# Performance work log

Hardware: AMD Instinct MI355X
Metric: run time of the kernel (lower is better)

Reference implementation:

```python
import jax, jax.numpy as jnp
import numpy as np

B, L, D = 8, 2048, 1024


def setup_inputs() -> dict:
    key = jax.random.key(0)
    kq, kk, kv, km = jax.random.split(key, 4)
    q = jax.random.normal(kq, (B, L, D), dtype=jnp.float32)
    k = jax.random.normal(kk, (B, L, D), dtype=jnp.float32)
    v = jax.random.normal(kv, (B, L, D), dtype=jnp.float32)
    rep_mask = jax.random.randint(km, (B, L, 1), 0, 2, dtype=jnp.int32)
    return {"q": q, "k": k, "v": v, "rep_mask": rep_mask}


def reference(q, k, v, rep_mask):
    # rep_mask: (B, L, 1) binary -> tiled pair mask (B, L, L)
    b, l, _ = rep_mask.shape
    m = rep_mask.astype(jnp.float32)
    mask = m.reshape(b, l, 1) * m.reshape(b, 1, l)  # (B, L, L)

    # scores: (B, L1, L2)
    attn = jnp.einsum('bqd,bkd->bqk', q, k)

    # custom masked softmax (faithful to original: mask applied pre-max and post-exp)
    masked_vec = attn * mask
    max_vec = jnp.max(masked_vec, axis=2, keepdims=True)
    masked_exps = jnp.exp(masked_vec - max_vec) * mask
    masked_sums = jnp.sum(masked_exps, axis=2, keepdims=True)
    masked_sums = masked_sums + (masked_sums == 0).astype(jnp.float32)  # avoid 0/0 rows
    attn = masked_exps / (masked_sums + 1e-20)

    out = jnp.einsum('bqk,bkd->bqd', attn, v)
    return out
```

## Files before the change

### kernel.cpp

```cpp
#include <hip/hip_runtime.h>
#include <cstdint>
#include <cstddef>

#define BB 8
#define LL 2048
#define DD 1024
#define KT 8

typedef _Float16 f16;
typedef _Float16 f16x4 __attribute__((ext_vector_type(4)));
typedef _Float16 f16x8 __attribute__((ext_vector_type(8)));
typedef float f32x4 __attribute__((ext_vector_type(4)));

__device__ __forceinline__ void gload_lds16(const void* g, void* l) {
  __builtin_amdgcn_global_load_lds(
      (const __attribute__((address_space(1))) void*)g,
      (__attribute__((address_space(3))) void*)l, 16, 0, 0);
}

__global__ void cvt_kernel(const float* __restrict__ src, f16* __restrict__ dst, int n) {
  const int t = blockIdx.x * blockDim.x + threadIdx.x;
  const int stride = gridDim.x * blockDim.x;
  for (int i = t * 4; i < n; i += stride * 4) {
    const float4 v = *(const float4*)(src + i);
    f16x4 o;
    o[0] = (f16)v.x; o[1] = (f16)v.y; o[2] = (f16)v.z; o[3] = (f16)v.w;
    *(f16x4*)(dst + i) = o;
  }
}

__global__ void vtrans_kernel(const float* __restrict__ v, f16* __restrict__ vt) {
  __shared__ float tile[32][33];
  const int b = blockIdx.z;
  const int k0 = blockIdx.x * 32, d0 = blockIdx.y * 32;
  const int tx = threadIdx.x & 31, ty0 = threadIdx.x >> 5;
#pragma unroll
  for (int i = 0; i < 4; ++i) {
    int ty = ty0 + i * 8;
    tile[ty][tx] = v[((size_t)b * LL + k0 + ty) * DD + d0 + tx];
  }
  __syncthreads();
#pragma unroll
  for (int i = 0; i < 4; ++i) {
    int ty = ty0 + i * 8;
    vt[((size_t)b * DD + d0 + ty) * LL + k0 + tx] = (f16)tile[tx][ty];
  }
}

template <int MODE>
__global__ __launch_bounds__(256, 2) void qk_kernel(
    const f16* __restrict__ Q16, const f16* __restrict__ K16,
    const int* __restrict__ rep, float* __restrict__ part,
    const float* __restrict__ MR, f16* __restrict__ P16) {
  __shared__ __align__(16) f16 Qs[64 * 32];
  __shared__ __align__(16) f16 Ks[256 * 32];
  __shared__ float mrow[64];
  __shared__ float mcol[256];
  __shared__ float MRs[128];
  __shared__ float pm[256];
  __shared__ float pz[256];

  const int kt = blockIdx.x, qt = blockIdx.y, b = blockIdx.z;
  const int q0 = qt * 64, k0 = kt * 256;
  const int tid = threadIdx.x;
  const int w = tid >> 6, l = tid & 63;

  mcol[tid] = (float)rep[(size_t)b * LL + k0 + tid];
  if (tid < 64) mrow[tid] = (float)rep[(size_t)b * LL + q0 + tid];
  if (MODE == 1 && tid < 128) MRs[tid] = MR[((size_t)b * LL + q0) * 2 + tid];

  const int rl = l >> 2, jc = l & 3;
  const int jsrc = jc ^ ((rl >> 1) & 3);
  const f16* qsrc = Q16 + ((size_t)b * LL + q0 + w * 16 + rl) * DD + jsrc * 8;
  const f16* ksrc = K16 + ((size_t)b * LL + k0 + w * 64 + rl) * DD + jsrc * 8;

  f32x4 acc[4][4] = {};
  const int lo16 = l & 15, hi = l >> 4;

  for (int ds = 0; ds < 32; ++ds) {
    gload_lds16(qsrc + ds * 32, &Qs[w * 16 * 32]);
    gload_lds16(ksrc + ds * 32,            &Ks[(w * 64) * 32]);
    gload_lds16(ksrc + 16 * DD + ds * 32,  &Ks[(w * 64 + 16) * 32]);
    gload_lds16(ksrc + 32 * DD + ds * 32,  &Ks[(w * 64 + 32) * 32]);
    gload_lds16(ksrc + 48 * DD + ds * 32,  &Ks[(w * 64 + 48) * 32]);
    __syncthreads();
    f16x8 af[4];
#pragma unroll
    for (int qf = 0; qf < 4; ++qf) {
      int r = qf * 16 + lo16;
      af[qf] = *(const f16x8*)&Qs[r * 32 + ((hi ^ ((r >> 1) & 3)) << 3)];
    }
#pragma unroll
    for (int kf = 0; kf < 4; ++kf) {
      int rk = w * 64 + kf * 16 + lo16;
      f16x8 bf = *(const f16x8*)&Ks[rk * 32 + ((hi ^ ((rk >> 1) & 3)) << 3)];
#pragma unroll
      for (int qf = 0; qf < 4; ++qf)
        acc[qf][kf] = __builtin_amdgcn_mfma_f32_16x16x32_f16(af[qf], bf, acc[qf][kf], 0, 0, 0);
    }
    __syncthreads();
  }

  float mkv[4];
#pragma unroll
  for (int kf = 0; kf < 4; ++kf) mkv[kf] = mcol[w * 64 + kf * 16 + lo16];

  if (MODE == 0) {
#pragma unroll
    for (int qf = 0; qf < 4; ++qf) {
#pragma unroll
      for (int r = 0; r < 4; ++r) {
        const int row = qf * 16 + hi * 4 + r;
        const float mqv = mrow[row];
        float v0 = acc[qf][0][r] * mqv * mkv[0];
        float v1 = acc[qf][1][r] * mqv * mkv[1];
        float v2 = acc[qf][2][r] * mqv * mkv[2];
        float v3 = acc[qf][3][r] * mqv * mkv[3];
        float mx = fmaxf(fmaxf(v0, v1), fmaxf(v2, v3));
#pragma unroll
        for (int s = 1; s < 16; s <<= 1) mx = fmaxf(mx, __shfl_xor(mx, s, 64));
        float zz = 0.f;
        zz += (mqv * mkv[0] != 0.f) ? __expf(v0 - mx) : 0.f;
        zz += (mqv * mkv[1] != 0.f) ? __expf(v1 - mx) : 0.f;
        zz += (mqv * mkv[2] != 0.f) ? __expf(v2 - mx) : 0.f;
        zz += (mqv * mkv[3] != 0.f) ? __expf(v3 - mx) : 0.f;
#pragma unroll
        for (int s = 1; s < 16; s <<= 1) zz += __shfl_xor(zz, s, 64);
        if (lo16 == 0) { pm[w * 64 + row] = mx; pz[w * 64 + row] = zz; }
      }
    }
    __syncthreads();
    if (tid < 64) {
      float m0 = pm[tid], m1 = pm[64 + tid], m2 = pm[128 + tid], m3 = pm[192 + tid];
      float M4 = fmaxf(fmaxf(m0, m1), fmaxf(m2, m3));
      float Z4 = pz[tid] * __expf(m0 - M4) + pz[64 + tid] * __expf(m1 - M4) +
                 pz[128 + tid] * __expf(m2 - M4) + pz[192 + tid] * __expf(m3 - M4);
      size_t base = (((size_t)b * LL + q0 + tid) * KT + kt) * 2;
      part[base] = M4;
      part[base + 1] = Z4;
    }
  } else {
#pragma unroll
    for (int qf = 0; qf < 4; ++qf) {
#pragma unroll
      for (int r = 0; r < 4; ++r) {
        const int row = qf * 16 + hi * 4 + r;
        const float mqv = mrow[row];
        const float Mv = MRs[row * 2], Rv = MRs[row * 2 + 1];
#pragma unroll
        for (int kf = 0; kf < 4; ++kf) {
          float p = 0.f;
          if (mqv * mkv[kf] != 0.f) p = __expf(acc[qf][kf][r] - Mv) * Rv;
          P16[((size_t)b * LL + q0 + row) * LL + (k0 + w * 64 + kf * 16 + lo16)] = (f16)p;
        }
      }
    }
  }
}

__global__ void combine_kernel(const float* __restrict__ part, float* __restrict__ MR) {
  const int row = blockIdx.x * blockDim.x + threadIdx.x;
  const float* p = part + (size_t)row * KT * 2;
  float M = p[0];
#pragma unroll
  for (int t = 1; t < KT; ++t) M = fmaxf(M, p[2 * t]);
  float Z = 0.f;
#pragma unroll
  for (int t = 0; t < KT; ++t) Z += p[2 * t + 1] * __expf(p[2 * t] - M);
  float Zf = Z + ((Z == 0.f) ? 1.f : 0.f) + 1e-20f;
  MR[(size_t)row * 2] = M;
  MR[(size_t)row * 2 + 1] = 1.f / Zf;
}

__global__ __launch_bounds__(256, 2) void pv_kernel(
    const f16* __restrict__ P16, const f16* __restrict__ V16T, float* __restrict__ out) {
  __shared__ __align__(16) f16 Ps[64 * 32];
  __shared__ __align__(16) f16 Vs[4][64 * 32];
  const int dt = blockIdx.x, qt = blockIdx.y, b = blockIdx.z;
  const int q0 = qt * 64, d0 = dt * 256;
  const int tid = threadIdx.x, w = tid >> 6, l = tid & 63;
  const int rl = l >> 2, jc = l & 3, jsrc = jc ^ ((rl >> 1) & 3);
  const int lo16 = l & 15, hi = l >> 4;

  const f16* psrc = P16 + ((size_t)b * LL + q0 + w * 16 + rl) * LL + jsrc * 8;
  const f16* vsrc = V16T + ((size_t)b * DD + d0 + w * 64 + rl) * LL + jsrc * 8;

  f32x4 acc[4][4] = {};

  for (int ks = 0; ks < 64; ++ks) {
    gload_lds16(psrc + ks * 32, &Ps[w * 16 * 32]);
    gload_lds16(vsrc + ks * 32,           &Vs[w][0]);
    gload_lds16(vsrc + 16 * LL + ks * 32, &Vs[w][16 * 32]);
    gload_lds16(vsrc + 32 * LL + ks * 32, &Vs[w][32 * 32]);
    gload_lds16(vsrc + 48 * LL + ks * 32, &Vs[w][48 * 32]);
    __syncthreads();
    f16x8 af[4];
#pragma unroll
    for (int qf = 0; qf < 4; ++qf) {
      int r = qf * 16 + lo16;
      af[qf] = *(const f16x8*)&Ps[r * 32 + ((hi ^ ((r >> 1) & 3)) << 3)];
    }
#pragma unroll
    for (int df = 0; df < 4; ++df) {
      int rv = df * 16 + lo16;
      f16x8 bf = *(const f16x8*)&Vs[w][rv * 32 + ((hi ^ ((rv >> 1) & 3)) << 3)];
#pragma unroll
      for (int qf = 0; qf < 4; ++qf)
        acc[qf][df] = __builtin_amdgcn_mfma_f32_16x16x32_f16(af[qf], bf, acc[qf][df], 0, 0, 0);
    }
    __syncthreads();
  }
#pragma unroll
  for (int qf = 0; qf < 4; ++qf)
#pragma unroll
    for (int df = 0; df < 4; ++df)
#pragma unroll
      for (int r = 0; r < 4; ++r) {
        int row = qf * 16 + hi * 4 + r;
        int col = d0 + w * 64 + df * 16 + lo16;
        out[((size_t)b * LL + q0 + row) * DD + col] = acc[qf][df][r];
      }
}

extern "C" void kernel_launch(void* const* d_in, const int* in_sizes, int n_in,
                              void* d_out, int out_size, void* d_ws, size_t ws_size,
                              hipStream_t stream) {
  const float* q = (const float*)d_in[0];
  const float* k = (const float*)d_in[1];
  const float* v = (const float*)d_in[2];
  const int* rep = (const int*)d_in[3];
  float* out = (float*)d_out;

  char* ws = (char*)d_ws;
  f16* Q16 = (f16*)(ws);
  f16* K16 = (f16*)(ws + 33554432);
  f16* V16T = (f16*)(ws + 67108864);
  f16* P16 = (f16*)(ws + 100663296);
  float* part = (float*)(ws + 167772160);
  float* MR = (float*)(ws + 168820736);

  const int n = BB * LL * DD;
  cvt_kernel<<<2048, 256, 0, stream>>>(q, Q16, n);
  cvt_kernel<<<2048, 256, 0, stream>>>(k, K16, n);
  vtrans_kernel<<<dim3(LL / 32, DD / 32, BB), 256, 0, stream>>>(v, V16T);
  qk_kernel<0><<<dim3(KT, LL / 64, BB), 256, 0, stream>>>(Q16, K16, rep, part, nullptr, nullptr);
  combine_kernel<<<BB * LL / 256, 256, 0, stream>>>(part, MR);
  qk_kernel<1><<<dim3(KT, LL / 64, BB), 256, 0, stream>>>(Q16, K16, rep, nullptr, MR, P16);
  pv_kernel<<<dim3(DD / 256, LL / 64, BB), 256, 0, stream>>>(P16, V16T, out);
}
```

Measured before the change: 526.9 us.

## Fuse QK passes with tile-local softmax and rescale in PV; double-buffer loads

The second QK GEMM pass is removed. The single QK kernel now writes exp(score minus the tile-local max) to P16, along with per-tile max and sum partials. The PV kernel computes a per-row, per-key-tile correction factor from the partials and the combined max/reciprocal-sum, and multiplies the P fragments by it before the MFMA. Both GEMM loops also gain double-buffered LDS staging, so the next K-slice load overlaps the current compute. This saves a full QK GEMM, at the cost of extra LDS, an extra reduction barrier, and f16 rounding of the correction factors.

```diff
diff --git a/kernel.cpp b/kernel.cpp
--- a/kernel.cpp
+++ b/kernel.cpp
@@ -47,18 +47,17 @@
   }
 }
 
-template <int MODE>
 __global__ __launch_bounds__(256, 2) void qk_kernel(
     const f16* __restrict__ Q16, const f16* __restrict__ K16,
     const int* __restrict__ rep, float* __restrict__ part,
-    const float* __restrict__ MR, f16* __restrict__ P16) {
-  __shared__ __align__(16) f16 Qs[64 * 32];
-  __shared__ __align__(16) f16 Ks[256 * 32];
+    f16* __restrict__ P16) {
+  __shared__ __align__(16) f16 Qs[2][64 * 32];
+  __shared__ __align__(16) f16 Ks[2][256 * 32];
   __shared__ float mrow[64];
   __shared__ float mcol[256];
-  __shared__ float MRs[128];
   __shared__ float pm[256];
   __shared__ float pz[256];
+  __shared__ float mr64[64];
 
   const int kt = blockIdx.x, qt = blockIdx.y, b = blockIdx.z;
   const int q0 = qt * 64, k0 = kt * 256;
@@ -67,7 +66,6 @@
 
   mcol[tid] = (float)rep[(size_t)b * LL + k0 + tid];
   if (tid < 64) mrow[tid] = (float)rep[(size_t)b * LL + q0 + tid];
-  if (MODE == 1 && tid < 128) MRs[tid] = MR[((size_t)b * LL + q0) * 2 + tid];
 
   const int rl = l >> 2, jc = l & 3;
   const int jsrc = jc ^ ((rl >> 1) & 3);
@@ -77,84 +75,94 @@
   f32x4 acc[4][4] = {};
   const int lo16 = l & 15, hi = l >> 4;
 
+  auto stage = [&](int buf, int ds) {
+    gload_lds16(qsrc + ds * 32, &Qs[buf][w * 16 * 32]);
+    gload_lds16(ksrc + ds * 32,           &Ks[buf][(w * 64) * 32]);
+    gload_lds16(ksrc + 16 * DD + ds * 32, &Ks[buf][(w * 64 + 16) * 32]);
+    gload_lds16(ksrc + 32 * DD + ds * 32, &Ks[buf][(w * 64 + 32) * 32]);
+    gload_lds16(ksrc + 48 * DD + ds * 32, &Ks[buf][(w * 64 + 48) * 32]);
+  };
+
+  stage(0, 0);
+  __syncthreads();
+  int cur = 0;
   for (int ds = 0; ds < 32; ++ds) {
-    gload_lds16(qsrc + ds * 32, &Qs[w * 16 * 32]);
-    gload_lds16(ksrc + ds * 32,            &Ks[(w * 64) * 32]);
-    gload_lds16(ksrc + 16 * DD + ds * 32,  &Ks[(w * 64 + 16) * 32]);
-    gload_lds16(ksrc + 32 * DD + ds * 32,  &Ks[(w * 64 + 32) * 32]);
-    gload_lds16(ksrc + 48 * DD + ds * 32,  &Ks[(w * 64 + 48) * 32]);
-    __syncthreads();
+    if (ds < 31) stage(cur ^ 1, ds + 1);
     f16x8 af[4];
 #pragma unroll
     for (int qf = 0; qf < 4; ++qf) {
       int r = qf * 16 + lo16;
-      af[qf] = *(const f16x8*)&Qs[r * 32 + ((hi ^ ((r >> 1) & 3)) << 3)];
+      af[qf] = *(const f16x8*)&Qs[cur][r * 32 + ((hi ^ ((r >> 1) & 3)) << 3)];
     }
 #pragma unroll
     for (int kf = 0; kf < 4; ++kf) {
       int rk = w * 64 + kf * 16 + lo16;
-      f16x8 bf = *(const f16x8*)&Ks[rk * 32 + ((hi ^ ((rk >> 1) & 3)) << 3)];
+      f16x8 bf = *(const f16x8*)&Ks[cur][rk * 32 + ((hi ^ ((rk >> 1) & 3)) << 3)];
 #pragma unroll
       for (int qf = 0; qf < 4; ++qf)
         acc[qf][kf] = __builtin_amdgcn_mfma_f32_16x16x32_f16(af[qf], bf, acc[qf][kf], 0, 0, 0);
     }
     __syncthreads();
+    cur ^= 1;
   }
 
   float mkv[4];
 #pragma unroll
   for (int kf = 0; kf < 4; ++kf) mkv[kf] = mcol[w * 64 + kf * 16 + lo16];
 
-  if (MODE == 0) {
-#pragma unroll
-    for (int qf = 0; qf < 4; ++qf) {
-#pragma unroll
-      for (int r = 0; r < 4; ++r) {
-        const int row = qf * 16 + hi * 4 + r;
-        const float mqv = mrow[row];
-        float v0 = acc[qf][0][r] * mqv * mkv[0];
-        float v1 = acc[qf][1][r] * mqv * mkv[1];
-        float v2 = acc[qf][2][r] * mqv * mkv[2];
-        float v3 = acc[qf][3][r] * mqv * mkv[3];
-        float mx = fmaxf(fmaxf(v0, v1), fmaxf(v2, v3));
-#pragma unroll
-        for (int s = 1; s < 16; s <<= 1) mx = fmaxf(mx, __shfl_xor(mx, s, 64));
-        float zz = 0.f;
-        zz += (mqv * mkv[0] != 0.f) ? __expf(v0 - mx) : 0.f;
-        zz += (mqv * mkv[1] != 0.f) ? __expf(v1 - mx) : 0.f;
-        zz += (mqv * mkv[2] != 0.f) ? __expf(v2 - mx) : 0.f;
-        zz += (mqv * mkv[3] != 0.f) ? __expf(v3 - mx) : 0.f;
-#pragma unroll
-        for (int s = 1; s < 16; s <<= 1) zz += __shfl_xor(zz, s, 64);
-        if (lo16 == 0) { pm[w * 64 + row] = mx; pz[w * 64 + row] = zz; }
-      }
-    }
-    __syncthreads();
-    if (tid < 64) {
-      float m0 = pm[tid], m1 = pm[64 + tid], m2 = pm[128 + tid], m3 = pm[192 + tid];
-      float M4 = fmaxf(fmaxf(m0, m1), fmaxf(m2, m3));
-      float Z4 = pz[tid] * __expf(m0 - M4) + pz[64 + tid] * __expf(m1 - M4) +
-                 pz[128 + tid] * __expf(m2 - M4) + pz[192 + tid] * __expf(m3 - M4);
-      size_t base = (((size_t)b * LL + q0 + tid) * KT + kt) * 2;
-      part[base] = M4;
-      part[base + 1] = Z4;
-    }
-  } else {
-#pragma unroll
-    for (int qf = 0; qf < 4; ++qf) {
-#pragma unroll
-      for (int r = 0; r < 4; ++r) {
-        const int row = qf * 16 + hi * 4 + r;
-        const float mqv = mrow[row];
-        const float Mv = MRs[row * 2], Rv = MRs[row * 2 + 1];
-#pragma unroll
-        for (int kf = 0; kf < 4; ++kf) {
-          float p = 0.f;
-          if (mqv * mkv[kf] != 0.f) p = __expf(acc[qf][kf][r] - Mv) * Rv;
-          P16[((size_t)b * LL + q0 + row) * LL + (k0 + w * 64 + kf * 16 + lo16)] = (f16)p;
-        }
-      }
-    }
+#pragma unroll
+  for (int qf = 0; qf < 4; ++qf) {
+#pragma unroll
+    for (int r = 0; r < 4; ++r) {
+      const int row = qf * 16 + hi * 4 + r;
+      const float mqv = mrow[row];
+      float v0 = acc[qf][0][r] * mqv * mkv[0];
+      float v1 = acc[qf][1][r] * mqv * mkv[1];
+      float v2 = acc[qf][2][r] * mqv * mkv[2];
+      float v3 = acc[qf][3][r] * mqv * mkv[3];
+      float mx = fmaxf(fmaxf(v0, v1), fmaxf(v2, v3));
+#pragma unroll
+      for (int s = 1; s < 16; s <<= 1) mx = fmaxf(mx, __shfl_xor(mx, s, 64));
+      if (lo16 == 0) pm[w * 64 + row] = mx;
+    }
+  }
+  __syncthreads();
+  if (tid < 64)
+    mr64[tid] = fmaxf(fmaxf(pm[tid], pm[64 + tid]), fmaxf(pm[128 + tid], pm[192 + tid]));
+  __syncthreads();
+
+#pragma unroll
+  for (int qf = 0; qf < 4; ++qf) {
+#pragma unroll
+    for (int r = 0; r < 4; ++r) {
+      const int row = qf * 16 + hi * 4 + r;
+      const float mqv = mrow[row];
+      const float Mv = mr64[row];
+      float v0 = acc[qf][0][r] * mqv * mkv[0];
+      float v1 = acc[qf][1][r] * mqv * mkv[1];
+      float v2 = acc[qf][2][r] * mqv * mkv[2];
+      float v3 = acc[qf][3][r] * mqv * mkv[3];
+      float e0 = (mqv * mkv[0] != 0.f) ? __expf(v0 - Mv) : 0.f;
+      float e1 = (mqv * mkv[1] != 0.f) ? __expf(v1 - Mv) : 0.f;
+      float e2 = (mqv * mkv[2] != 0.f) ? __expf(v2 - Mv) : 0.f;
+      float e3 = (mqv * mkv[3] != 0.f) ? __expf(v3 - Mv) : 0.f;
+      const size_t prow = ((size_t)b * LL + q0 + row) * LL + k0 + w * 64 + lo16;
+      P16[prow] = (f16)e0;
+      P16[prow + 16] = (f16)e1;
+      P16[prow + 32] = (f16)e2;
+      P16[prow + 48] = (f16)e3;
+      float zz = e0 + e1 + e2 + e3;
+#pragma unroll
+      for (int s = 1; s < 16; s <<= 1) zz += __shfl_xor(zz, s, 64);
+      if (lo16 == 0) pz[w * 64 + row] = zz;
+    }
+  }
+  __syncthreads();
+  if (tid < 64) {
+    float Z4 = pz[tid] + pz[64 + tid] + pz[128 + tid] + pz[192 + tid];
+    size_t base = (((size_t)b * LL + q0 + tid) * KT + kt) * 2;
+    part[base] = mr64[tid];
+    part[base + 1] = Z4;
   }
 }
 
@@ -173,42 +181,69 @@
 }
 
 __global__ __launch_bounds__(256, 2) void pv_kernel(
-    const f16* __restrict__ P16, const f16* __restrict__ V16T, float* __restrict__ out) {
-  __shared__ __align__(16) f16 Ps[64 * 32];
-  __shared__ __align__(16) f16 Vs[4][64 * 32];
+    const f16* __restrict__ P16, const f16* __restrict__ V16T,
+    const float* __restrict__ part, const float* __restrict__ MR,
+    float* __restrict__ out) {
+  __shared__ __align__(16) f16 Ps[2][64 * 32];
+  __shared__ __align__(16) f16 Vs[2][4 * 64 * 32];
+  __shared__ float cS[64][9];
+
   const int dt = blockIdx.x, qt = blockIdx.y, b = blockIdx.z;
   const int q0 = qt * 64, d0 = dt * 256;
   const int tid = threadIdx.x, w = tid >> 6, l = tid & 63;
   const int rl = l >> 2, jc = l & 3, jsrc = jc ^ ((rl >> 1) & 3);
   const int lo16 = l & 15, hi = l >> 4;
 
+  for (int i = tid; i < 512; i += 256) {
+    const int r = i >> 3, t = i & 7;
+    const size_t grow = (size_t)b * LL + q0 + r;
+    const float Mt = part[(grow * KT + t) * 2];
+    const float Mg = MR[grow * 2], Rg = MR[grow * 2 + 1];
+    cS[r][t] = __expf(Mt - Mg) * Rg;
+  }
+
   const f16* psrc = P16 + ((size_t)b * LL + q0 + w * 16 + rl) * LL + jsrc * 8;
   const f16* vsrc = V16T + ((size_t)b * DD + d0 + w * 64 + rl) * LL + jsrc * 8;
 
+  auto stage = [&](int buf, int ks) {
+    gload_lds16(psrc + ks * 32, &Ps[buf][w * 16 * 32]);
+    gload_lds16(vsrc + ks * 32,           &Vs[buf][w * 64 * 32]);
+    gload_lds16(vsrc + 16 * LL + ks * 32, &Vs[buf][(w * 64 + 16) * 32]);
+    gload_lds16(vsrc + 32 * LL + ks * 32, &Vs[buf][(w * 64 + 32) * 32]);
+    gload_lds16(vsrc + 48 * LL + ks * 32, &Vs[buf][(w * 64 + 48) * 32]);
+  };
+
   f32x4 acc[4][4] = {};
-
-  for (int ks = 0; ks < 64; ++ks) {
-    gload_lds16(psrc + ks * 32, &Ps[w * 16 * 32]);
-    gload_lds16(vsrc + ks * 32,           &Vs[w][0]);
-    gload_lds16(vsrc + 16 * LL + ks * 32, &Vs[w][16 * 32]);
-    gload_lds16(vsrc + 32 * LL + ks * 32, &Vs[w][32 * 32]);
-    gload_lds16(vsrc + 48 * LL + ks * 32, &Vs[w][48 * 32]);
-    __syncthreads();
-    f16x8 af[4];
-#pragma unroll
-    for (int qf = 0; qf < 4; ++qf) {
-      int r = qf * 16 + lo16;
-      af[qf] = *(const f16x8*)&Ps[r * 32 + ((hi ^ ((r >> 1) & 3)) << 3)];
-    }
-#pragma unroll
-    for (int df = 0; df < 4; ++df) {
-      int rv = df * 16 + lo16;
-      f16x8 bf = *(const f16x8*)&Vs[w][rv * 32 + ((hi ^ ((rv >> 1) & 3)) << 3)];
-#pragma unroll
-      for (int qf = 0; qf < 4; ++qf)
-        acc[qf][df] = __builtin_amdgcn_mfma_f32_16x16x32_f16(af[qf], bf, acc[qf][df], 0, 0, 0);
-    }
-    __syncthreads();
+  stage(0, 0);
+  __syncthreads();
+  int cur = 0;
+  for (int kt2 = 0; kt2 < 8; ++kt2) {
+    f16 ct[4];
+#pragma unroll
+    for (int qf = 0; qf < 4; ++qf) ct[qf] = (f16)cS[qf * 16 + lo16][kt2];
+    for (int ki = 0; ki < 8; ++ki) {
+      const int ks = kt2 * 8 + ki;
+      if (ks < 63) stage(cur ^ 1, ks + 1);
+      f16x8 af[4];
+#pragma unroll
+      for (int qf = 0; qf < 4; ++qf) {
+        int r = qf * 16 + lo16;
+        af[qf] = *(const f16x8*)&Ps[cur][r * 32 + ((hi ^ ((r >> 1) & 3)) << 3)];
+        const f16 c = ct[qf];
+        f16x8 cv = {c, c, c, c, c, c, c, c};
+        af[qf] = af[qf] * cv;
+      }
+#pragma unroll
+      for (int df = 0; df < 4; ++df) {
+        int rv = w * 64 + df * 16 + lo16;
+        f16x8 bf = *(const f16x8*)&Vs[cur][rv * 32 + ((hi ^ ((rv >> 1) & 3)) << 3)];
+#pragma unroll
+        for (int qf = 0; qf < 4; ++qf)
+          acc[qf][df] = __builtin_amdgcn_mfma_f32_16x16x32_f16(af[qf], bf, acc[qf][df], 0, 0, 0);
+      }
+      __syncthreads();
+      cur ^= 1;
+    }
   }
 #pragma unroll
   for (int qf = 0; qf < 4; ++qf)
@@ -243,8 +278,7 @@
   cvt_kernel<<<2048, 256, 0, stream>>>(q, Q16, n);
   cvt_kernel<<<2048, 256, 0, stream>>>(k, K16, n);
   vtrans_kernel<<<dim3(LL / 32, DD / 32, BB), 256, 0, stream>>>(v, V16T);
-  qk_kernel<0><<<dim3(KT, LL / 64, BB), 256, 0, stream>>>(Q16, K16, rep, part, nullptr, nullptr);
+  qk_kernel<<<dim3(KT, LL / 64, BB), 256, 0, stream>>>(Q16, K16, rep, part, P16);
   combine_kernel<<<BB * LL / 256, 256, 0, stream>>>(part, MR);
-  qk_kernel<1><<<dim3(KT, LL / 64, BB), 256, 0, stream>>>(Q16, K16, rep, nullptr, MR, P16);
-  pv_kernel<<<dim3(DD / 256, LL / 64, BB), 256, 0, stream>>>(P16, V16T, out);
-}
+  pv_kernel<<<dim3(DD / 256, LL / 64, BB), 256, 0, stream>>>(P16, V16T, part, MR, out);
+}
```

New measurement: 476.8 us. -9.5%, faster.
